# Kernel tuning notes

Hardware: AMD Instinct MI355X
Metric: run time of the kernel (lower is better)

## Reference

```python
import jax, jax.numpy as jnp
import numpy as np

NUM_HEADS = 16
NUM_KV_HEADS = 4
HEAD_DIM = 64
ROPE_BASE = 10000.0


def _rope(x, pos0):
    # x: [b, s, n, h_d]; interleaved-pair RoPE (torchtune RotaryPositionalEmbeddings)
    b, s, n, hd = x.shape
    half = hd // 2
    inv_freq = 1.0 / (ROPE_BASE ** (jnp.arange(0, hd, 2, dtype=jnp.float32) / hd))  # [half]
    t = jnp.arange(s, dtype=jnp.float32) + pos0                                      # [s]
    freqs = t[:, None] * inv_freq[None, :]                                           # [s, half]
    cos = jnp.cos(freqs)[None, :, None, :].astype(x.dtype)
    sin = jnp.sin(freqs)[None, :, None, :].astype(x.dtype)
    xr = x.reshape(b, s, n, half, 2)
    x1, x2 = xr[..., 0], xr[..., 1]
    o1 = x1 * cos - x2 * sin
    o2 = x1 * sin + x2 * cos
    return jnp.stack([o1, o2], axis=-1).reshape(b, s, n, hd)


def setup_inputs() -> dict:
    key = jax.random.key(0)
    k1, k2, k3 = jax.random.split(key, 3)
    b, s, d = 2, 2048, 1024
    qkv_dim = (NUM_HEADS + 2 * NUM_KV_HEADS) * HEAD_DIM  # 1536
    x = jax.random.normal(k1, (b, s, d), dtype=jnp.float32)
    Wqkv = jax.random.normal(k2, (d, qkv_dim), dtype=jnp.float32) * (d ** -0.5)
    Wo = jax.random.normal(k3, (d, d), dtype=jnp.float32) * (d ** -0.5)
    return {"x": x, "Wqkv": Wqkv, "Wo": Wo, "curr_pos": 0}


def reference(x, Wqkv, Wo, curr_pos):
    b, s, d = x.shape
    n_h, n_kv, hd = NUM_HEADS, NUM_KV_HEADS, HEAD_DIM
    q_per_kv = n_h // n_kv
    total_qkv = q_per_kv + 2

    # fused QKV projection then split per kv group
    qkv = (x @ Wqkv).reshape(b, s, n_kv, total_qkv, hd)
    q = qkv[:, :, :, :q_per_kv]            # [b, s, n_kv, q_per_kv, hd]
    k = qkv[:, :, :, q_per_kv:q_per_kv + 1]  # [b, s, n_kv, 1, hd]
    v = qkv[:, :, :, q_per_kv + 1:]          # [b, s, n_kv, 1, hd]

    # GQA expand k/v to match query heads, then flatten heads
    k = jnp.broadcast_to(k, (b, s, n_kv, q_per_kv, hd))
    v = jnp.broadcast_to(v, (b, s, n_kv, q_per_kv, hd))
    q = q.reshape(b, s, n_h, hd)
    k = k.reshape(b, s, n_h, hd)
    v = v.reshape(b, s, n_h, hd)

    # RoPE on q and k
    q = _rope(q, curr_pos)
    k = _rope(k, curr_pos)

    # causal SDPA (kv_cache is None -> is_causal=True, mask=None, dropout=0)
    scale = 1.0 / jnp.sqrt(jnp.asarray(hd, dtype=x.dtype))
    scores = jnp.einsum('bqhd,bkhd->bhqk', q, k) * scale  # [b, n_h, s, s]
    causal = jnp.tril(jnp.ones((s, s), dtype=bool))
    scores = jnp.where(causal[None, None], scores, jnp.finfo(scores.dtype).min)
    attn = jax.nn.softmax(scores, axis=-1)
    out = jnp.einsum('bhqk,bkhd->bqhd', attn, v).reshape(b, s, n_h * hd)
    return out @ Wo
```

## Files before the change

kernel.cpp:

```cpp
#include <hip/hip_runtime.h>
#include <hip/hip_bf16.h>

typedef __attribute__((ext_vector_type(8))) short bf16x8;
typedef __attribute__((ext_vector_type(4))) short bf16x4;
typedef __attribute__((ext_vector_type(4))) float f32x4;
typedef __attribute__((ext_vector_type(16))) float f32x16;
typedef unsigned short u16;
typedef unsigned int u32;

#define NH 16
#define NKV 4
#define HD 64
#define BB 2
#define SS 2048
#define DD 1024
#define QKVD 1536

#define QSCALE 0.18033688011112f
#define MBIAS  -12.0f

template<int V> struct IntC { static constexpr int value = V; };

__device__ __forceinline__ u16 f2b(float f){
  __hip_bfloat16 h = __float2bfloat16(f);
  u16 u; __builtin_memcpy(&u, &h, 2); return u;
}
__device__ __forceinline__ float b2f(u32 u){
  u <<= 16; float f; __builtin_memcpy(&f, &u, 4); return f;
}
__device__ __forceinline__ float exp2fast(float x){
#if __has_builtin(__builtin_amdgcn_exp2f)
  return __builtin_amdgcn_exp2f(x);
#else
  return exp2f(x);
#endif
}

__device__ __forceinline__ void gload16(const void* g, void* l){
  __builtin_amdgcn_global_load_lds((const __attribute__((address_space(1))) void*)g,
                                   (__attribute__((address_space(3))) void*)l, 16, 0, 0);
}

__global__ __launch_bounds__(256) void prep1(const float* __restrict__ x,
                                             u16* __restrict__ Xb,
                                             const float* __restrict__ Wqkv,
                                             u16* __restrict__ WqkvT,
                                             const float* __restrict__ Wo,
                                             u16* __restrict__ WoT){
  __shared__ u16 tile[64][65];
  const int bid = blockIdx.x;
  if (bid < 4096){
    int idx = (bid * 256 + threadIdx.x) * 4;
    float4 v = *(const float4*)(x + idx);
    u32 lo = (u32)f2b(v.x) | ((u32)f2b(v.y) << 16);
    u32 hi = (u32)f2b(v.z) | ((u32)f2b(v.w) << 16);
    *(uint2*)(Xb + idx) = make_uint2(lo, hi);
    return;
  }
  const float* in; u16* outT; int K, N, n0, k0;
  bool perm = false;
  if (bid < 4480){
    int id = bid - 4096; in = Wqkv; outT = WqkvT; K = 1024; N = 1536;
    n0 = (id % 24) * 64; k0 = (id / 24) * 64;
    perm = ((n0 >> 6) % 6) != 5;
  } else {
    int id = bid - 4480; in = Wo; outT = WoT; K = 1024; N = 1024;
    n0 = (id % 16) * 64; k0 = (id / 16) * 64;
  }
  int cr = threadIdx.x >> 6, cc = threadIdx.x & 63;
#pragma unroll
  for (int rr = 0; rr < 16; rr++){
    int row = rr * 4 + cr;
    tile[row][cc] = f2b(in[(size_t)(k0 + row) * N + n0 + cc]);
  }
  __syncthreads();
#pragma unroll
  for (int rr = 0; rr < 16; rr++){
    int d = rr * 4 + cr;
    int dn = perm ? ((d & 1) ? 32 + (d >> 1) : (d >> 1)) : d;
    outT[(size_t)(n0 + dn) * K + k0 + cc] = tile[cc][d];
  }
}

__global__ __launch_bounds__(256) void gemm_qkv(const __hip_bfloat16* __restrict__ A,
                                                const __hip_bfloat16* __restrict__ BT,
                                                const int* __restrict__ posp,
                                                u16* __restrict__ Qr,
                                                u16* __restrict__ Kr,
                                                u16* __restrict__ Vt){
  constexpr int Kd = 1024, N = 1536;
  __shared__ __align__(16) char smem[2][32768];
  int bid = blockIdx.x;
  const int cpx = gridDim.x >> 3;
  bid = (bid & 7) * cpx + (bid >> 3);
  const int ntn = N >> 7;
  const int tm = bid / ntn, tn = bid % ntn;
  const int m0 = tm << 7, n0 = tn << 7;
  const int lane = threadIdx.x & 63, w = threadIdx.x >> 6;
  const int g = lane >> 4, i = lane & 15;
  const int wr = w >> 1, wc = w & 1;
  f32x4 acc[4][4] = {};
  const int lrow = lane >> 3;
  const int lcol = ((lane & 7) ^ lrow) * 8;
  const __hip_bfloat16* ga = A  + (size_t)(m0 + w * 32 + lrow) * Kd + lcol;
  const __hip_bfloat16* gb = BT + (size_t)(n0 + w * 32 + lrow) * Kd + lcol;
  const int xr = (i & 7) << 4;

  auto stage = [&](int buf, int kt){
    char* As = smem[buf];
    char* Bs = As + 16384;
#pragma unroll
    for (int h = 0; h < 4; h++)
      gload16(ga + kt + (size_t)(h * 8) * Kd, As + w * 4096 + h * 1024);
#pragma unroll
    for (int h = 0; h < 4; h++)
      gload16(gb + kt + (size_t)(h * 8) * Kd, Bs + w * 4096 + h * 1024);
  };

  stage(0, 0);
  asm volatile("s_waitcnt vmcnt(0)");
  __syncthreads();
  int cur = 0;
  for (int kt = 0; kt < Kd; kt += 64){
    if (kt + 64 < Kd) stage(cur ^ 1, kt + 64);
    const char* As = smem[cur];
    const char* Bs = As + 16384;
    bf16x8 af[2][4], bfr[2][4];
#pragma unroll
    for (int kh = 0; kh < 2; kh++){
#pragma unroll
      for (int x = 0; x < 4; x++){
        af[kh][x]  = *(const bf16x8*)(As + (wr * 64 + x * 16 + i) * 128 + ((kh * 64 + g * 16) ^ xr));
        bfr[kh][x] = *(const bf16x8*)(Bs + (wc * 64 + x * 16 + i) * 128 + ((kh * 64 + g * 16) ^ xr));
      }
    }
    __builtin_amdgcn_s_setprio(1);
#pragma unroll
    for (int kh = 0; kh < 2; kh++)
#pragma unroll
      for (int mi = 0; mi < 4; mi++)
#pragma unroll
        for (int ni = 0; ni < 4; ni++)
          acc[mi][ni] = __builtin_amdgcn_mfma_f32_16x16x32_bf16(af[kh][mi], bfr[kh][ni], acc[mi][ni], 0, 0, 0);
    __builtin_amdgcn_s_setprio(0);
    asm volatile("s_waitcnt vmcnt(0)");
    __syncthreads();
    cur ^= 1;
  }

  const int h24 = tn * 2 + wc;
  const int kvh = h24 / 6, slot = h24 - kvh * 6;
  const int bi = m0 >> 11;
  const int s0 = (m0 & 2047) + wr * 64 + g * 4;
  if (slot == 5){
    u16* vb = Vt + (size_t)(bi * NKV + kvh) * 64 * SS;
#pragma unroll
    for (int mi = 0; mi < 4; mi++)
#pragma unroll
      for (int ni = 0; ni < 4; ni++){
        bf16x4 ov;
#pragma unroll
        for (int r = 0; r < 4; r++) ov[r] = (short)f2b(acc[mi][ni][r]);
        *(bf16x4*)(vb + (size_t)(ni * 16 + i) * SS + s0 + mi * 16) = ov;
      }
  } else {
    const bool isq = slot < 4;
    u16* dst0 = isq ? Qr + (size_t)(bi * NH + kvh * 4 + slot) * SS * 64
                    : Kr + (size_t)(bi * NKV + kvh) * SS * 64;
    const float scale = isq ? QSCALE : 1.f;
    const int pos0 = posp[0];
#pragma unroll
    for (int nn = 0; nn < 2; nn++){
      const int p = nn * 16 + i;
      const float invf = exp2fast(-(float)p * 0.4152410118609203f);
#pragma unroll
      for (int mi = 0; mi < 4; mi++)
#pragma unroll
        for (int r = 0; r < 4; r++){
          const int si = s0 + mi * 16 + r;
          float sn, cs;
          sincosf((float)(si + pos0) * invf, &sn, &cs);
          const float x1 = acc[mi][nn][r], x2 = acc[mi][nn + 2][r];
          const float o1 = (x1 * cs - x2 * sn) * scale;
          const float o2 = (x1 * sn + x2 * cs) * scale;
          *(u32*)(dst0 + (size_t)si * 64 + 2 * p) = (u32)f2b(o1) | ((u32)f2b(o2) << 16);
        }
    }
  }
}

template<int TN, typename OT>
__global__ __launch_bounds__(256) void gemm_db(const __hip_bfloat16* __restrict__ A,
                                               const __hip_bfloat16* __restrict__ BT,
                                               OT* __restrict__ C,
                                               int M, int N, int K){
  constexpr int NW = TN / 32;
  constexpr int ABYTES = 128 * 128;
  constexpr int BBYTES = TN * 128;
  __shared__ __align__(16) char smem[2][ABYTES + BBYTES];
  const int ntn = N / TN;
  int bid = blockIdx.x;
  const int cpx = gridDim.x >> 3;
  bid = (bid & 7) * cpx + (bid >> 3);
  const int tm = bid / ntn, tn = bid % ntn;
  const int m0 = tm << 7, n0 = tn * TN;
  const int lane = threadIdx.x & 63, w = threadIdx.x >> 6;
  const int g = lane >> 4, i = lane & 15;
  const int wr = w >> 1, wc = w & 1;
  f32x4 acc[4][NW] = {};
  const int lrow = lane >> 3;
  const int lcol = ((lane & 7) ^ lrow) * 8;
  const __hip_bfloat16* ga = A  + (size_t)(m0 + w * 32 + lrow) * K + lcol;
  const __hip_bfloat16* gb = BT + (size_t)(n0 + w * 8 + lrow) * K + lcol;
  const int xr = (i & 7) << 4;

  auto stage = [&](int buf, int kt){
    char* As = smem[buf];
    char* Bs = As + ABYTES;
#pragma unroll
    for (int h = 0; h < 4; h++)
      gload16(ga + kt + (size_t)(h * 8) * K, As + w * 4096 + h * 1024);
#pragma unroll
    for (int h = 0; h < NW; h++)
      gload16(gb + kt + (size_t)(h * 32) * K, Bs + (h * 4 + w) * 1024);
  };

  stage(0, 0);
  asm volatile("s_waitcnt vmcnt(0)");
  __syncthreads();
  int cur = 0;
  for (int kt = 0; kt < K; kt += 64){
    if (kt + 64 < K) stage(cur ^ 1, kt + 64);
    const char* As = smem[cur];
    const char* Bs = As + ABYTES;
    bf16x8 af[2][4], bfr[2][NW];
#pragma unroll
    for (int kh = 0; kh < 2; kh++){
#pragma unroll
      for (int x = 0; x < 4; x++)
        af[kh][x] = *(const bf16x8*)(As + (wr * 64 + x * 16 + i) * 128 + ((kh * 64 + g * 16) ^ xr));
#pragma unroll
      for (int n = 0; n < NW; n++)
        bfr[kh][n] = *(const bf16x8*)(Bs + (wc * (TN / 2) + n * 16 + i) * 128 + ((kh * 64 + g * 16) ^ xr));
    }
    __builtin_amdgcn_s_setprio(1);
#pragma unroll
    for (int kh = 0; kh < 2; kh++)
#pragma unroll
      for (int mi = 0; mi < 4; mi++)
#pragma unroll
        for (int ni = 0; ni < NW; ni++)
          acc[mi][ni] = __builtin_amdgcn_mfma_f32_16x16x32_bf16(af[kh][mi], bfr[kh][ni], acc[mi][ni], 0, 0, 0);
    __builtin_amdgcn_s_setprio(0);
    asm volatile("s_waitcnt vmcnt(0)");
    __syncthreads();
    cur ^= 1;
  }
#pragma unroll
  for (int mi = 0; mi < 4; mi++)
#pragma unroll
    for (int ni = 0; ni < NW; ni++){
      size_t base = (size_t)(m0 + wr * 64 + mi * 16 + g * 4) * N + n0 + wc * (TN / 2) + ni * 16 + i;
#pragma unroll
      for (int r = 0; r < 4; r++){
        float v = acc[mi][ni][r];
        if constexpr (sizeof(OT) == 2) C[base + (size_t)r * N] = (OT)f2b(v);
        else                           C[base + (size_t)r * N] = v;
      }
    }
}

__global__ __launch_bounds__(256) void attn_fwd(const __hip_bfloat16* __restrict__ Qr,
                                                const __hip_bfloat16* __restrict__ Kr,
                                                const __hip_bfloat16* __restrict__ Vt,
                                                u16* __restrict__ Ao){
  __shared__ __align__(16) char smem[2][16384];
  const int blk = blockIdx.x;
  const int qt = 15 - (blk >> 5);
  const int bh = blk & 31;
  const int hi = bh & 15;
  const int bi = bh >> 4;
  const int kvh = hi >> 2;
  const int tid = threadIdx.x;
  const int lane = tid & 63, w = tid >> 6;
  const int qr = lane & 31, hlf = lane >> 5;
  const int q0 = qt * 128 + w * 32;
  const int qabs = q0 + qr;
  const u16* Qp = (const u16*)Qr + (size_t)(bi * NH + hi) * SS * 64;
  const u16* Kp = (const u16*)Kr + (size_t)(bi * NKV + kvh) * SS * 64;
  const u16* Vp = (const u16*)Vt + (size_t)(bi * NKV + kvh) * 64 * SS;

  bf16x8 qb[4];
#pragma unroll
  for (int ks = 0; ks < 4; ks++)
    qb[ks] = *(const bf16x8*)(Qp + (size_t)(q0 + qr) * 64 + ks * 16 + hlf * 8);

  const int srow = tid >> 3;
  const int sw   = ((tid & 7) ^ (srow & 7)) * 8;
  const int xr   = (lane & 7) << 4;

  auto stage = [&](int buf, int j0){
#pragma unroll
    for (int n = 0; n < 2; n++)
      gload16(Kp + (size_t)(j0 + n * 32 + srow) * 64 + sw,
              &smem[buf][n * 4096 + tid * 16]);
#pragma unroll
    for (int n = 0; n < 2; n++)
      gload16(Vp + (size_t)(n * 32 + srow) * SS + j0 + sw,
              &smem[buf][8192 + n * 4096 + tid * 16]);
  };

  float l_row = 0.f;
  f32x16 o[2] = {};

  auto body = [&](auto modec, int buf, int j0){
    constexpr int MODE = decltype(modec)::value;
    if constexpr (MODE == 2){ if (w < 2) return; }
    const bool msk = (MODE == 1) ? (w < 2) : (MODE == 2);
    const char* Kb = smem[buf];
    const char* Vb = Kb + 8192;
    f32x16 st[2];
    __builtin_amdgcn_s_setprio(1);
#pragma unroll
    for (int jb = 0; jb < 2; jb++){
      f32x16 a = {MBIAS, MBIAS, MBIAS, MBIAS, MBIAS, MBIAS, MBIAS, MBIAS,
                  MBIAS, MBIAS, MBIAS, MBIAS, MBIAS, MBIAS, MBIAS, MBIAS};
      const int row = jb * 32 + qr;
#pragma unroll
      for (int ks = 0; ks < 4; ks++){
        bf16x8 kf = *(const bf16x8*)(Kb + row * 128 + ((ks * 32 + hlf * 16) ^ xr));
        a = __builtin_amdgcn_mfma_f32_32x32x16_bf16(kf, qb[ks], a, 0, 0, 0);
      }
      st[jb] = a;
    }
    __builtin_amdgcn_s_setprio(0);
    bf16x8 vA[2][4];
#pragma unroll
    for (int db = 0; db < 2; db++){
      const int row = db * 32 + qr;
#pragma unroll
      for (int ks = 0; ks < 4; ks++)
        vA[db][ks] = *(const bf16x8*)(Vb + row * 128 + ((ks * 32 + hlf * 16) ^ xr));
    }
    float lsum = 0.f;
#pragma unroll
    for (int jb = 0; jb < 2; jb++){
      float p[16];
#pragma unroll
      for (int r = 0; r < 16; r++){
        float e = exp2fast(st[jb][r]);
        if (msk){
          int jabs = j0 + jb * 32 + (r & 3) + 8 * (r >> 2) + 4 * hlf;
          e = (jabs > qabs) ? 0.f : e;
        }
        p[r] = e;
        lsum += e;
      }
      u32 c[8];
#pragma unroll
      for (int m = 0; m < 8; m++)
        asm("v_cvt_pk_bf16_f32 %0, %1, %2" : "=v"(c[m]) : "v"(p[2 * m]), "v"(p[2 * m + 1]));
      asm volatile("v_permlane32_swap_b32 %0, %1" : "+v"(c[0]), "+v"(c[2]));
      asm volatile("v_permlane32_swap_b32 %0, %1" : "+v"(c[1]), "+v"(c[3]));
      asm volatile("v_permlane32_swap_b32 %0, %1" : "+v"(c[4]), "+v"(c[6]));
      asm volatile("v_permlane32_swap_b32 %0, %1" : "+v"(c[5]), "+v"(c[7]));
      bf16x8 pfE, pfO;
      __builtin_memcpy(&pfE, &c[0], 16);
      __builtin_memcpy(&pfO, &c[4], 16);
      __builtin_amdgcn_s_setprio(1);
#pragma unroll
      for (int db = 0; db < 2; db++){
        o[db] = __builtin_amdgcn_mfma_f32_32x32x16_bf16(vA[db][jb * 2 + 0], pfE, o[db], 0, 0, 0);
        o[db] = __builtin_amdgcn_mfma_f32_32x32x16_bf16(vA[db][jb * 2 + 1], pfO, o[db], 0, 0, 0);
      }
      __builtin_amdgcn_s_setprio(0);
    }
    lsum += __shfl_xor(lsum, 32, 64);
    l_row += lsum;
  };

  stage(0, 0);
  asm volatile("s_waitcnt vmcnt(0)");
  __syncthreads();
  int cur = 0;
  const int nfull = 2 * qt;
  for (int t = 0; t < nfull; t++){
    stage(cur ^ 1, (t + 1) * 64);
    body(IntC<0>{}, cur, t * 64);
    asm volatile("s_waitcnt vmcnt(0)");
    __syncthreads();
    cur ^= 1;
  }
  stage(cur ^ 1, (nfull + 1) * 64);
  body(IntC<1>{}, cur, nfull * 64);
  asm volatile("s_waitcnt vmcnt(0)");
  __syncthreads();
  cur ^= 1;
  body(IntC<2>{}, cur, (nfull + 1) * 64);

  const float linv = 1.f / l_row;
  u16* orow = Ao + (size_t)(bi * SS + q0 + qr) * (NH * HD) + hi * 64 + hlf * 4;
#pragma unroll
  for (int db = 0; db < 2; db++)
#pragma unroll
    for (int tg = 0; tg < 4; tg++){
      bf16x4 ov;
#pragma unroll
      for (int r = 0; r < 4; r++) ov[r] = (short)f2b(o[db][tg * 4 + r] * linv);
      *(bf16x4*)(orow + db * 32 + tg * 8) = ov;
    }
}

extern "C" void kernel_launch(void* const* d_in, const int* in_sizes, int n_in,
                              void* d_out, int out_size, void* d_ws, size_t ws_size,
                              hipStream_t stream){
  const float* x    = (const float*)d_in[0];
  const float* Wqkv = (const float*)d_in[1];
  const float* Wo   = (const float*)d_in[2];
  const int*   pos  = (const int*)d_in[3];
  float* out = (float*)d_out;
  char* ws = (char*)d_ws;

  __hip_bfloat16* Xb    = (__hip_bfloat16*)(ws);
  __hip_bfloat16* WqkvT = (__hip_bfloat16*)(ws + 8388608);
  __hip_bfloat16* WoT   = (__hip_bfloat16*)(ws + 11534336);
  __hip_bfloat16* Qr    = (__hip_bfloat16*)(ws + 26214400);
  __hip_bfloat16* Kr    = (__hip_bfloat16*)(ws + 34603008);
  __hip_bfloat16* Vt    = (__hip_bfloat16*)(ws + 36700160);
  __hip_bfloat16* Ao    = (__hip_bfloat16*)(ws);

  prep1<<<4736, 256, 0, stream>>>(x, (u16*)Xb, Wqkv, (u16*)WqkvT, Wo, (u16*)WoT);
  gemm_qkv<<<384, 256, 0, stream>>>(Xb, WqkvT, pos, (u16*)Qr, (u16*)Kr, (u16*)Vt);
  attn_fwd<<<512, 256, 0, stream>>>(Qr, Kr, Vt, (u16*)Ao);
  gemm_db<64, float><<<512, 256, 0, stream>>>(Ao, WoT, out, 4096, 1024, 1024);
}
```

Before: 82.27 us.

## Stage 128-key tiles per barrier and skip fully masked diagonal sub-blocks

The attention kernel now loads two 64-key sub-tiles (128 keys) per pipeline stage into a doubled LDS buffer, which halves the number of waitcnt/syncthreads barriers across the KV loop. On the diagonal tiles it also skips the second 32-key QK and PV block for waves whose queries all lie before those keys, avoiding wasted MFMA and exp work. The cost is twice the LDS per block (64KB), which may lower occupancy, plus extra in-flight loads per stage.

```diff
diff --git a/kernel.cpp b/kernel.cpp
--- a/kernel.cpp
+++ b/kernel.cpp
@@ -274,7 +274,7 @@
                                                 const __hip_bfloat16* __restrict__ Kr,
                                                 const __hip_bfloat16* __restrict__ Vt,
                                                 u16* __restrict__ Ao){
-  __shared__ __align__(16) char smem[2][16384];
+  __shared__ __align__(16) char smem[2][2][16384];
   const int blk = blockIdx.x;
   const int qt = 15 - (blk >> 5);
   const int bh = blk & 31;
@@ -301,28 +301,33 @@
 
   auto stage = [&](int buf, int j0){
 #pragma unroll
-    for (int n = 0; n < 2; n++)
-      gload16(Kp + (size_t)(j0 + n * 32 + srow) * 64 + sw,
-              &smem[buf][n * 4096 + tid * 16]);
-#pragma unroll
-    for (int n = 0; n < 2; n++)
-      gload16(Vp + (size_t)(n * 32 + srow) * SS + j0 + sw,
-              &smem[buf][8192 + n * 4096 + tid * 16]);
+    for (int s = 0; s < 2; s++){
+#pragma unroll
+      for (int n = 0; n < 2; n++)
+        gload16(Kp + (size_t)(j0 + s * 64 + n * 32 + srow) * 64 + sw,
+                &smem[buf][s][n * 4096 + tid * 16]);
+#pragma unroll
+      for (int n = 0; n < 2; n++)
+        gload16(Vp + (size_t)(n * 32 + srow) * SS + j0 + s * 64 + sw,
+                &smem[buf][s][8192 + n * 4096 + tid * 16]);
+    }
   };
 
   float l_row = 0.f;
   f32x16 o[2] = {};
 
-  auto body = [&](auto modec, int buf, int j0){
+  auto body = [&](auto modec, int buf, int sub, int j0){
     constexpr int MODE = decltype(modec)::value;
     if constexpr (MODE == 2){ if (w < 2) return; }
     const bool msk = (MODE == 1) ? (w < 2) : (MODE == 2);
-    const char* Kb = smem[buf];
+    const bool skipjb1 = msk && !(w & 1);
+    const char* Kb = smem[buf][sub];
     const char* Vb = Kb + 8192;
     f32x16 st[2];
     __builtin_amdgcn_s_setprio(1);
 #pragma unroll
     for (int jb = 0; jb < 2; jb++){
+      if (jb == 1 && skipjb1) continue;
       f32x16 a = {MBIAS, MBIAS, MBIAS, MBIAS, MBIAS, MBIAS, MBIAS, MBIAS,
                   MBIAS, MBIAS, MBIAS, MBIAS, MBIAS, MBIAS, MBIAS, MBIAS};
       const int row = jb * 32 + qr;
@@ -345,6 +350,7 @@
     float lsum = 0.f;
 #pragma unroll
     for (int jb = 0; jb < 2; jb++){
+      if (jb == 1 && skipjb1) continue;
       float p[16];
 #pragma unroll
       for (int r = 0; r < 16; r++){
@@ -383,20 +389,16 @@
   asm volatile("s_waitcnt vmcnt(0)");
   __syncthreads();
   int cur = 0;
-  const int nfull = 2 * qt;
-  for (int t = 0; t < nfull; t++){
-    stage(cur ^ 1, (t + 1) * 64);
-    body(IntC<0>{}, cur, t * 64);
+  for (int t = 0; t < qt; t++){
+    stage(cur ^ 1, (t + 1) * 128);
+    body(IntC<0>{}, cur, 0, t * 128);
+    body(IntC<0>{}, cur, 1, t * 128 + 64);
     asm volatile("s_waitcnt vmcnt(0)");
     __syncthreads();
     cur ^= 1;
   }
-  stage(cur ^ 1, (nfull + 1) * 64);
-  body(IntC<1>{}, cur, nfull * 64);
-  asm volatile("s_waitcnt vmcnt(0)");
-  __syncthreads();
-  cur ^= 1;
-  body(IntC<2>{}, cur, (nfull + 1) * 64);
+  body(IntC<1>{}, cur, 0, qt * 128);
+  body(IntC<2>{}, cur, 1, qt * 128 + 64);
 
   const float linv = 1.f / l_row;
   u16* orow = Ao + (size_t)(bi * SS + q0 + qr) * (NH * HD) + hi * 64 + hlf * 4;
```

New measurement: 79.97 us. 1.03x faster.
